# Performance work log

Hardware: AMD Instinct MI355X
Metric: run time of the kernel (lower is better)

## Reference

```python
import jax, jax.numpy as jnp
import numpy as np

M = 50000
N = 50000
H = 32
C = 128
K = 15          # sum(shell_sizes) = 1 + 14
GROUPS = 8
CPG = C // GROUPS  # 16
RADIUS = 1.2
SIGMA = 0.9
INF = 1.0e6


def _make_kernel_points():
    # fixed='center': first point at origin, rest uniformly in the ball of radius RADIUS
    rng = np.random.RandomState(42)
    pts = rng.randn(K, 3).astype(np.float32)
    pts /= np.linalg.norm(pts, axis=1, keepdims=True) + 1e-9
    r = rng.rand(K, 1).astype(np.float32) ** (1.0 / 3.0)
    pts = pts * r * RADIUS
    pts[0] = 0.0
    return jnp.asarray(pts)


def setup_inputs() -> dict:
    key = jax.random.key(0)
    ks = jax.random.split(key, 8)
    q_pts = jax.random.normal(ks[0], (M, 3), jnp.float32) * 5.0
    s_pts = q_pts + 0.0  # M == N case (same point set)
    s_feats = jax.random.normal(ks[1], (N, C), jnp.float32)
    neighb_inds = jax.random.randint(ks[2], (M, H), 0, N)
    da_scale = jax.random.uniform(ks[3], (M,), jnp.float32, 0.5, 1.5)
    # learned params
    weights = jax.random.normal(ks[4], (K, C), jnp.float32) * (1.0 / np.sqrt(C))
    w1 = jax.random.normal(ks[5], (C, C), jnp.float32) * (1.0 / np.sqrt(C))
    b1 = jnp.zeros((C,), jnp.float32)
    w2 = jax.random.normal(ks[6], (C, K * CPG), jnp.float32) * (1.0 / np.sqrt(C))
    kernel_points = _make_kernel_points()
    return {
        "q_pts": q_pts, "s_pts": s_pts, "s_feats": s_feats,
        "neighb_inds": neighb_inds, "da_scale": da_scale,
        "weights": weights, "w1": w1, "b1": b1, "w2": w2,
        "kernel_points": kernel_points,
    }


def reference(q_pts, s_pts, s_feats, neighb_inds, da_scale,
              weights, w1, b1, w2, kernel_points):
    # --- neighbor feature gather (padded shadow row of zeros) ---
    padded = jnp.concatenate([s_feats, jnp.zeros((1, C), s_feats.dtype)], axis=0)
    neighbor_feats = padded[neighb_inds]               # [M, H, C]

    # --- modulations from pooled feats (M == N -> pooled = s_feats) ---
    pooled = s_feats
    h = jax.nn.leaky_relu(pooled @ w1 + b1, 0.1)
    modulations = jax.nn.sigmoid(h @ w2)               # [M, K*CPG]
    modulations = modulations.reshape(-1, K, CPG, 1)
    conv_w = weights.reshape(1, K, CPG, GROUPS) * modulations
    conv_w = conv_w.reshape(-1, K, C)                  # [M, K, C]

    # --- density-adaptive kernel-point influences (no-grad in original) ---
    s_pad = jnp.concatenate([s_pts, jnp.full((1, 3), INF, s_pts.dtype)], axis=0)
    neighbors = s_pad[neighb_inds] - q_pts[:, None, :]            # [M, H, 3]
    scaled_kp = kernel_points[None] * da_scale[:, None, None]     # [M, K, 3]
    diff = neighbors[:, :, None, :] - scaled_kp[:, None, :, :]    # [M, H, K, 3]
    sq_d = jnp.sum(diff * diff, axis=-1)                          # [M, H, K]
    nn_sq = jnp.min(sq_d, axis=2)                                 # [M, H]
    nn_idx = jnp.argmin(sq_d, axis=2)                             # [M, H]
    infl = jnp.clip(1.0 - jnp.sqrt(nn_sq) / SIGMA, 0.0)           # linear mode
    infl = jax.lax.stop_gradient(infl)

    # --- gather per-neighbor kernel weights, modulate, aggregate ---
    nw = jnp.take_along_axis(conv_w, nn_idx[:, :, None], axis=1)  # [M, H, C]
    nw = nw * infl[:, :, None]
    return jnp.sum(neighbor_feats * nw, axis=1)                   # [M, C]
```

## Files before the change

### kernel.cpp

```cpp
#include <hip/hip_runtime.h>
#include <cstddef>
#include <cstdint>

namespace {
constexpr int H_N    = 32;
constexpr int C_F    = 128;
constexpr int K_P    = 15;
constexpr int MODC   = 240;
constexpr int ROWS_B = 64;
constexpr int X_OFF   = 0;
constexpr int MOD_OFF = 16384;
constexpr int LDS_SZ  = 16384 + ROWS_B * MODC * 2;
}

typedef __attribute__((ext_vector_type(8))) short short8v;
typedef __attribute__((ext_vector_type(4))) float f32x4;

__device__ __forceinline__ unsigned short bf16_hi(float f) {
    unsigned u = __builtin_bit_cast(unsigned, f);
    unsigned r = (u + 0x7FFFu + ((u >> 16) & 1u)) >> 16;
    return (unsigned short)r;
}
__device__ __forceinline__ float bf16_f(unsigned short h) {
    unsigned u = ((unsigned)h) << 16;
    return __builtin_bit_cast(float, u);
}

__global__ __launch_bounds__(256)
void split_w_kernel(const float* __restrict__ w1, const float* __restrict__ w2,
                    unsigned short* __restrict__ w1t, unsigned short* __restrict__ w2t)
{
    const int i = blockIdx.x * 256 + threadIdx.x;
    if (i < C_F * C_F) {
        const int c = i >> 7, j = i & 127;
        w1t[j * C_F + c] = bf16_hi(w1[i]);
    }
    const int i2 = i - C_F * C_F;
    if (i2 >= 0 && i2 < C_F * MODC) {
        const int c = i2 / MODC, j = i2 - c * MODC;
        w2t[j * C_F + c] = bf16_hi(w2[i2]);
    }
}

__global__ __launch_bounds__(512, 2)
void fused_kernel(const float* __restrict__ q_pts,
                  const float* __restrict__ s_pts,
                  const float* __restrict__ s_feats,
                  const int* __restrict__ nbi,
                  const float* __restrict__ da_scale,
                  const float* __restrict__ weights,
                  const float* __restrict__ kp,
                  const unsigned short* __restrict__ w1t,
                  const unsigned short* __restrict__ w2t,
                  const float* __restrict__ b1,
                  float* __restrict__ out,
                  int M)
{
    __shared__ __align__(16) unsigned char lds[LDS_SZ];

    const int t  = threadIdx.x;
    const int r0 = blockIdx.x * ROWS_B;
    const int rows = min(M - r0, ROWS_B);

    {
        const int row = t >> 3;
        const int k0  = (t & 7) << 4;
        const float4* src = reinterpret_cast<const float4*>(
            s_feats + (size_t)(r0 + row) * C_F + k0);
        #pragma unroll
        for (int s = 0; s < 2; ++s) {
            float v[8];
            if (row < rows) {
                const float4 a = src[s * 2 + 0];
                const float4 b = src[s * 2 + 1];
                v[0] = a.x; v[1] = a.y; v[2] = a.z; v[3] = a.w;
                v[4] = b.x; v[5] = b.y; v[6] = b.z; v[7] = b.w;
            } else {
                #pragma unroll
                for (int e = 0; e < 8; ++e) v[e] = 0.f;
            }
            short8v hv;
            #pragma unroll
            for (int e = 0; e < 8; ++e) hv[e] = (short)bf16_hi(v[e]);
            const unsigned addr = (unsigned)((row * 256 + (k0 + s * 8) * 2) ^ ((row & 7) << 4));
            *reinterpret_cast<short8v*>(lds + X_OFF + addr) = hv;
        }
    }
    __syncthreads();

    const int wave = t >> 6, lane = t & 63;
    const int wc = wave;
    const int g  = lane >> 4;
    const int ln = lane & 15;

    {
        const int col = wc * 16 + ln;
        f32x4 acc[4];
        {
            const float b = b1[col];
            #pragma unroll
            for (int rt = 0; rt < 4; ++rt) acc[rt] = f32x4{b, b, b, b};
        }
        #pragma unroll
        for (int ks = 0; ks < 4; ++ks) {
            short8v a[4];
            #pragma unroll
            for (int rt = 0; rt < 4; ++rt) {
                const int row = rt * 16 + ln;
                const unsigned addr = (unsigned)((row * 256 + (ks * 32 + g * 8) * 2) ^ ((row & 7) << 4));
                a[rt] = *reinterpret_cast<const short8v*>(lds + X_OFF + addr);
            }
            const short8v b = *reinterpret_cast<const short8v*>(
                w1t + (size_t)col * C_F + ks * 32 + g * 8);
            #pragma unroll
            for (int rt = 0; rt < 4; ++rt)
                acc[rt] = __builtin_amdgcn_mfma_f32_16x16x32_bf16(a[rt], b, acc[rt], 0, 0, 0);
        }
        __syncthreads();

        #pragma unroll
        for (int rt = 0; rt < 4; ++rt) {
            #pragma unroll
            for (int r = 0; r < 4; ++r) {
                float v = acc[rt][r];
                v = v > 0.f ? v : 0.1f * v;
                const int row = rt * 16 + g * 4 + r;
                const unsigned addr = (unsigned)((row * 256 + col * 2) ^ ((row & 7) << 4));
                *reinterpret_cast<unsigned short*>(lds + X_OFF + addr) = bf16_hi(v);
            }
        }
    }
    __syncthreads();

    {
        f32x4 acc2[4][2];
        #pragma unroll
        for (int rt = 0; rt < 4; ++rt)
            #pragma unroll
            for (int cs = 0; cs < 2; ++cs) acc2[rt][cs] = f32x4{0.f, 0.f, 0.f, 0.f};

        #pragma unroll
        for (int ks = 0; ks < 4; ++ks) {
            short8v a[4];
            #pragma unroll
            for (int rt = 0; rt < 4; ++rt) {
                const int row = rt * 16 + ln;
                const unsigned addr = (unsigned)((row * 256 + (ks * 32 + g * 8) * 2) ^ ((row & 7) << 4));
                a[rt] = *reinterpret_cast<const short8v*>(lds + X_OFF + addr);
            }
            #pragma unroll
            for (int cs = 0; cs < 2; ++cs) {
                const int ctile = wc + 8 * cs;
                if (ctile < K_P) {
                    const int col = ctile * 16 + ln;
                    const short8v b = *reinterpret_cast<const short8v*>(
                        w2t + (size_t)col * C_F + ks * 32 + g * 8);
                    #pragma unroll
                    for (int rt = 0; rt < 4; ++rt)
                        acc2[rt][cs] = __builtin_amdgcn_mfma_f32_16x16x32_bf16(a[rt], b, acc2[rt][cs], 0, 0, 0);
                }
            }
        }

        #pragma unroll
        for (int rt = 0; rt < 4; ++rt) {
            #pragma unroll
            for (int cs = 0; cs < 2; ++cs) {
                const int ctile = wc + 8 * cs;
                if (ctile < K_P) {
                    const int col = ctile * 16 + ln;
                    #pragma unroll
                    for (int r = 0; r < 4; ++r) {
                        const int row = rt * 16 + g * 4 + r;
                        const float v = 1.f / (1.f + __expf(-acc2[rt][cs][r]));
                        *reinterpret_cast<unsigned short*>(
                            lds + MOD_OFF + row * (MODC * 2) + col * 2) = bf16_hi(v);
                    }
                }
            }
        }
    }
    __syncthreads();

    for (int i = 0; i < 8; ++i) {
        const int ql = i * 8 + wave;
        if (ql >= rows) continue;
        const int mq = r0 + ql;

        const float qx = q_pts[mq * 3 + 0];
        const float qy = q_pts[mq * 3 + 1];
        const float qz = q_pts[mq * 3 + 2];
        const float das = da_scale[mq];

        int   idx = 0, nn = 0;
        float fl  = 0.f;
        if (lane < H_N) {
            idx = nbi[(size_t)mq * H_N + lane];
            const float sx = s_pts[idx * 3 + 0];
            const float sy = s_pts[idx * 3 + 1];
            const float sz = s_pts[idx * 3 + 2];
            const float dx = __fsub_rn(sx, qx);
            const float dy = __fsub_rn(sy, qy);
            const float dz = __fsub_rn(sz, qz);
            const float dd = __fadd_rn(__fadd_rn(__fmul_rn(dx, dx), __fmul_rn(dy, dy)),
                                       __fmul_rn(dz, dz));
            const float reach = 0.9f + 1.2f * das;
            if (dd < reach * reach) {
                float best = 3.4e38f; int bi = 0;
                #pragma unroll
                for (int k = 0; k < K_P; ++k) {
                    const float ex = __fsub_rn(dx, __fmul_rn(kp[k * 3 + 0], das));
                    const float ey = __fsub_rn(dy, __fmul_rn(kp[k * 3 + 1], das));
                    const float ez = __fsub_rn(dz, __fmul_rn(kp[k * 3 + 2], das));
                    const float d2 = __fadd_rn(__fadd_rn(__fmul_rn(ex, ex), __fmul_rn(ey, ey)),
                                               __fmul_rn(ez, ez));
                    if (d2 < best) { best = d2; bi = k; }
                }
                const float f = 1.f - sqrtf(best) / 0.9f;
                fl = fmaxf(f, 0.f);
                nn = bi;
            }
        }

        unsigned long long mask = __ballot(fl > 0.f);
        const int c0 = lane << 1;
        float2 acc = {0.f, 0.f};
        while (mask) {
            const int hb = __builtin_ctzll(mask);
            mask &= mask - 1;
            const int   ih = __shfl(idx, hb);
            const int   nh = __shfl(nn, hb);
            const float fh = __shfl(fl, hb);
            const float2 fv = *reinterpret_cast<const float2*>(s_feats + (size_t)ih * C_F + c0);
            const float2 wv = *reinterpret_cast<const float2*>(weights + nh * C_F + c0);
            const float  mv = bf16_f(*reinterpret_cast<const unsigned short*>(
                lds + MOD_OFF + ql * (MODC * 2) + (nh * 16 + (lane >> 2)) * 2));
            const float  s  = fh * mv;
            acc.x = fmaf(fv.x * wv.x, s, acc.x);
            acc.y = fmaf(fv.y * wv.y, s, acc.y);
        }
        reinterpret_cast<float2*>(out + (size_t)mq * C_F)[lane] = acc;
    }
}

extern "C" void kernel_launch(void* const* d_in, const int* in_sizes, int n_in,
                              void* d_out, int out_size, void* d_ws, size_t ws_size,
                              hipStream_t stream)
{
    const float* q_pts  = (const float*)d_in[0];
    const float* s_pts  = (const float*)d_in[1];
    const float* s_feat = (const float*)d_in[2];
    const int*   nbi    = (const int*)d_in[3];
    const float* da     = (const float*)d_in[4];
    const float* wts    = (const float*)d_in[5];
    const float* w1     = (const float*)d_in[6];
    const float* b1     = (const float*)d_in[7];
    const float* w2     = (const float*)d_in[8];
    const float* kp     = (const float*)d_in[9];
    float* out = (float*)d_out;

    const int M = in_sizes[4];

    unsigned short* w1t = (unsigned short*)d_ws;
    unsigned short* w2t = w1t + C_F * C_F;

    const int nsplit = (C_F * C_F + C_F * MODC + 255) / 256;
    split_w_kernel<<<dim3(nsplit), 256, 0, stream>>>(w1, w2, w1t, w2t);

    const int nb = (M + ROWS_B - 1) / ROWS_B;
    fused_kernel<<<dim3(nb), 512, 0, stream>>>(
        q_pts, s_pts, s_feat, nbi, da, wts, kp, w1t, w2t, b1, out, M);
}
```

Measured before the change: 46.83 us.

## Alias LDS buffers, raise occupancy, process two queries per wave

The modulation buffer now reuses the same LDS region as the bf16 feature tile. The sigmoid results stay in registers across a barrier before being written, which shrinks LDS per block so launch bounds can request 4 blocks per CU instead of 2. The gather stage now handles two query rows per wave, one per half-wave, with float4 loads instead of float2, so all 64 lanes do neighbor-influence work instead of 32. The risks are more register pressure under the tighter launch bound, and a serialized while loop because both halves share one ballot-driven iteration count.

```diff
diff --git a/kernel.cpp b/kernel.cpp
--- a/kernel.cpp
+++ b/kernel.cpp
@@ -8,9 +8,7 @@
 constexpr int K_P    = 15;
 constexpr int MODC   = 240;
 constexpr int ROWS_B = 64;
-constexpr int X_OFF   = 0;
-constexpr int MOD_OFF = 16384;
-constexpr int LDS_SZ  = 16384 + ROWS_B * MODC * 2;
+constexpr int LDS_SZ  = ROWS_B * MODC * 2;
 }
 
 typedef __attribute__((ext_vector_type(8))) short short8v;
@@ -42,7 +40,7 @@
     }
 }
 
-__global__ __launch_bounds__(512, 2)
+__global__ __launch_bounds__(512, 4)
 void fused_kernel(const float* __restrict__ q_pts,
                   const float* __restrict__ s_pts,
                   const float* __restrict__ s_feats,
@@ -83,7 +81,7 @@
             #pragma unroll
             for (int e = 0; e < 8; ++e) hv[e] = (short)bf16_hi(v[e]);
             const unsigned addr = (unsigned)((row * 256 + (k0 + s * 8) * 2) ^ ((row & 7) << 4));
-            *reinterpret_cast<short8v*>(lds + X_OFF + addr) = hv;
+            *reinterpret_cast<short8v*>(lds + addr) = hv;
         }
     }
     __syncthreads();
@@ -108,7 +106,7 @@
             for (int rt = 0; rt < 4; ++rt) {
                 const int row = rt * 16 + ln;
                 const unsigned addr = (unsigned)((row * 256 + (ks * 32 + g * 8) * 2) ^ ((row & 7) << 4));
-                a[rt] = *reinterpret_cast<const short8v*>(lds + X_OFF + addr);
+                a[rt] = *reinterpret_cast<const short8v*>(lds + addr);
             }
             const short8v b = *reinterpret_cast<const short8v*>(
                 w1t + (size_t)col * C_F + ks * 32 + g * 8);
@@ -126,76 +124,84 @@
                 v = v > 0.f ? v : 0.1f * v;
                 const int row = rt * 16 + g * 4 + r;
                 const unsigned addr = (unsigned)((row * 256 + col * 2) ^ ((row & 7) << 4));
-                *reinterpret_cast<unsigned short*>(lds + X_OFF + addr) = bf16_hi(v);
-            }
-        }
-    }
-    __syncthreads();
-
-    {
-        f32x4 acc2[4][2];
-        #pragma unroll
-        for (int rt = 0; rt < 4; ++rt)
-            #pragma unroll
-            for (int cs = 0; cs < 2; ++cs) acc2[rt][cs] = f32x4{0.f, 0.f, 0.f, 0.f};
-
-        #pragma unroll
-        for (int ks = 0; ks < 4; ++ks) {
-            short8v a[4];
-            #pragma unroll
-            for (int rt = 0; rt < 4; ++rt) {
-                const int row = rt * 16 + ln;
-                const unsigned addr = (unsigned)((row * 256 + (ks * 32 + g * 8) * 2) ^ ((row & 7) << 4));
-                a[rt] = *reinterpret_cast<const short8v*>(lds + X_OFF + addr);
-            }
-            #pragma unroll
-            for (int cs = 0; cs < 2; ++cs) {
-                const int ctile = wc + 8 * cs;
-                if (ctile < K_P) {
-                    const int col = ctile * 16 + ln;
-                    const short8v b = *reinterpret_cast<const short8v*>(
-                        w2t + (size_t)col * C_F + ks * 32 + g * 8);
-                    #pragma unroll
-                    for (int rt = 0; rt < 4; ++rt)
-                        acc2[rt][cs] = __builtin_amdgcn_mfma_f32_16x16x32_bf16(a[rt], b, acc2[rt][cs], 0, 0, 0);
+                *reinterpret_cast<unsigned short*>(lds + addr) = bf16_hi(v);
+            }
+        }
+    }
+    __syncthreads();
+
+    f32x4 acc2[4][2];
+    #pragma unroll
+    for (int rt = 0; rt < 4; ++rt)
+        #pragma unroll
+        for (int cs = 0; cs < 2; ++cs) acc2[rt][cs] = f32x4{0.f, 0.f, 0.f, 0.f};
+
+    #pragma unroll
+    for (int ks = 0; ks < 4; ++ks) {
+        short8v a[4];
+        #pragma unroll
+        for (int rt = 0; rt < 4; ++rt) {
+            const int row = rt * 16 + ln;
+            const unsigned addr = (unsigned)((row * 256 + (ks * 32 + g * 8) * 2) ^ ((row & 7) << 4));
+            a[rt] = *reinterpret_cast<const short8v*>(lds + addr);
+        }
+        #pragma unroll
+        for (int cs = 0; cs < 2; ++cs) {
+            const int ctile = wc + 8 * cs;
+            if (ctile < K_P) {
+                const int col = ctile * 16 + ln;
+                const short8v b = *reinterpret_cast<const short8v*>(
+                    w2t + (size_t)col * C_F + ks * 32 + g * 8);
+                #pragma unroll
+                for (int rt = 0; rt < 4; ++rt)
+                    acc2[rt][cs] = __builtin_amdgcn_mfma_f32_16x16x32_bf16(a[rt], b, acc2[rt][cs], 0, 0, 0);
+            }
+        }
+    }
+    #pragma unroll
+    for (int rt = 0; rt < 4; ++rt)
+        #pragma unroll
+        for (int cs = 0; cs < 2; ++cs)
+            #pragma unroll
+            for (int r = 0; r < 4; ++r)
+                acc2[rt][cs][r] = 1.f / (1.f + __expf(-acc2[rt][cs][r]));
+
+    __syncthreads();
+
+    #pragma unroll
+    for (int rt = 0; rt < 4; ++rt) {
+        #pragma unroll
+        for (int cs = 0; cs < 2; ++cs) {
+            const int ctile = wc + 8 * cs;
+            if (ctile < K_P) {
+                const int col = ctile * 16 + ln;
+                #pragma unroll
+                for (int r = 0; r < 4; ++r) {
+                    const int row = rt * 16 + g * 4 + r;
+                    *reinterpret_cast<unsigned short*>(
+                        lds + row * (MODC * 2) + col * 2) = bf16_hi(acc2[rt][cs][r]);
                 }
             }
         }
-
-        #pragma unroll
-        for (int rt = 0; rt < 4; ++rt) {
-            #pragma unroll
-            for (int cs = 0; cs < 2; ++cs) {
-                const int ctile = wc + 8 * cs;
-                if (ctile < K_P) {
-                    const int col = ctile * 16 + ln;
-                    #pragma unroll
-                    for (int r = 0; r < 4; ++r) {
-                        const int row = rt * 16 + g * 4 + r;
-                        const float v = 1.f / (1.f + __expf(-acc2[rt][cs][r]));
-                        *reinterpret_cast<unsigned short*>(
-                            lds + MOD_OFF + row * (MODC * 2) + col * 2) = bf16_hi(v);
-                    }
-                }
-            }
-        }
-    }
-    __syncthreads();
-
-    for (int i = 0; i < 8; ++i) {
-        const int ql = i * 8 + wave;
-        if (ql >= rows) continue;
+    }
+    __syncthreads();
+
+    const int hl   = lane & 31;
+    const int half = lane >> 5;
+    const int c0   = hl << 2;
+    for (int i = 0; i < 4; ++i) {
+        const int ql = i * 16 + wave * 2 + half;
+        const bool valid = ql < rows;
         const int mq = r0 + ql;
-
-        const float qx = q_pts[mq * 3 + 0];
-        const float qy = q_pts[mq * 3 + 1];
-        const float qz = q_pts[mq * 3 + 2];
-        const float das = da_scale[mq];
 
         int   idx = 0, nn = 0;
         float fl  = 0.f;
-        if (lane < H_N) {
-            idx = nbi[(size_t)mq * H_N + lane];
+        if (valid) {
+            const float qx = q_pts[mq * 3 + 0];
+            const float qy = q_pts[mq * 3 + 1];
+            const float qz = q_pts[mq * 3 + 2];
+            const float das = da_scale[mq];
+            idx = nbi[(size_t)mq * H_N + hl];
             const float sx = s_pts[idx * 3 + 0];
             const float sy = s_pts[idx * 3 + 1];
             const float sz = s_pts[idx * 3 + 2];
@@ -222,24 +228,28 @@
             }
         }
 
-        unsigned long long mask = __ballot(fl > 0.f);
-        const int c0 = lane << 1;
-        float2 acc = {0.f, 0.f};
-        while (mask) {
-            const int hb = __builtin_ctzll(mask);
-            mask &= mask - 1;
+        const unsigned long long mask = __ballot(fl > 0.f);
+        unsigned long long mymask = half ? (mask & 0xFFFFFFFF00000000ull)
+                                         : (mask & 0x00000000FFFFFFFFull);
+        float4 acc = {0.f, 0.f, 0.f, 0.f};
+        while (mymask) {
+            const int hb = __builtin_ctzll(mymask);
+            mymask &= mymask - 1;
             const int   ih = __shfl(idx, hb);
             const int   nh = __shfl(nn, hb);
             const float fh = __shfl(fl, hb);
-            const float2 fv = *reinterpret_cast<const float2*>(s_feats + (size_t)ih * C_F + c0);
-            const float2 wv = *reinterpret_cast<const float2*>(weights + nh * C_F + c0);
+            const float4 fv = *reinterpret_cast<const float4*>(s_feats + (size_t)ih * C_F + c0);
+            const float4 wv = *reinterpret_cast<const float4*>(weights + nh * C_F + c0);
             const float  mv = bf16_f(*reinterpret_cast<const unsigned short*>(
-                lds + MOD_OFF + ql * (MODC * 2) + (nh * 16 + (lane >> 2)) * 2));
+                lds + ql * (MODC * 2) + (nh * 16 + (hl >> 1)) * 2));
             const float  s  = fh * mv;
             acc.x = fmaf(fv.x * wv.x, s, acc.x);
             acc.y = fmaf(fv.y * wv.y, s, acc.y);
-        }
-        reinterpret_cast<float2*>(out + (size_t)mq * C_F)[lane] = acc;
+            acc.z = fmaf(fv.z * wv.z, s, acc.z);
+            acc.w = fmaf(fv.w * wv.w, s, acc.w);
+        }
+        if (valid)
+            *reinterpret_cast<float4*>(out + (size_t)mq * C_F + c0) = acc;
     }
 }
 
```

New measurement: 42.83 us. -8.5%, faster.
